# Kernel optimization log

Hardware: AMD Instinct MI355X
Metric: run time of the kernel (lower is better)

The kernel has to match this reference:

```python
import jax, jax.numpy as jnp
import numpy as np

N_NODES = 50000
N_EDGES = 800000
D_IN = 128
D_HID = 128
D_OUT = 128
N_GRAPHS = 512


def _linear_params(key, d_in, d_out):
    kw, kb = jax.random.split(key)
    bound = 1.0 / np.sqrt(d_in)
    W = jax.random.uniform(kw, (d_in, d_out), minval=-bound, maxval=bound, dtype=jnp.float32)
    b = jax.random.uniform(kb, (d_out,), minval=-bound, maxval=bound, dtype=jnp.float32)
    return W, b


def setup_inputs() -> dict:
    key = jax.random.key(0)
    ks = jax.random.split(key, 8)
    x = jax.random.normal(ks[0], (N_NODES, D_IN), dtype=jnp.float32)
    edge_index = jax.random.randint(ks[1], (2, N_EDGES), 0, N_NODES, dtype=jnp.int64)
    batch = jnp.sort(jax.random.randint(ks[2], (N_NODES,), 0, N_GRAPHS, dtype=jnp.int64))
    W1a, b1a = _linear_params(ks[3], D_IN, D_HID)
    W1b, b1b = _linear_params(ks[4], D_HID, D_HID)
    W2a, b2a = _linear_params(ks[5], D_HID, D_HID)
    W2b, b2b = _linear_params(ks[6], D_HID, D_OUT)
    Wfc, bfc = _linear_params(ks[7], D_OUT, D_OUT)
    return {"x": x, "edge_index": edge_index, "batch": batch,
            "W1a": W1a, "b1a": b1a, "W1b": W1b, "b1b": b1b,
            "W2a": W2a, "b2a": b2a, "W2b": W2b, "b2b": b2b,
            "Wfc": Wfc, "bfc": bfc}


def _gin_conv(h, src, dst, Wa, ba, Wb, bb):
    # neighbor sum: gather source features, scatter-add to targets (eps=0)
    agg = jax.ops.segment_sum(h[src], dst, num_segments=N_NODES)
    z = h + agg  # (1+eps)*x + sum_neighbors, eps=0
    z = jax.nn.relu(z @ Wa + ba)
    return z @ Wb + bb


def reference(x, edge_index, batch, W1a, b1a, W1b, b1b, W2a, b2a, W2b, b2b, Wfc, bfc):
    src, dst = edge_index[0], edge_index[1]
    h = jax.nn.relu(_gin_conv(x, src, dst, W1a, b1a, W1b, b1b))
    h = jax.nn.relu(_gin_conv(h, src, dst, W2a, b2a, W2b, b2b))
    g = jax.ops.segment_sum(h, batch, num_segments=N_GRAPHS)  # global_add_pool
    return jax.nn.relu(g @ Wfc + bfc)
```

## Files before the change

### kernel.cpp

```cpp
#include <hip/hip_runtime.h>

#define N_NODES 50000
#define N_EDGES 800000
#define N_GRAPHS 512
#define CAP 48

typedef __bf16 bf16x8 __attribute__((ext_vector_type(8)));
typedef float f32x4 __attribute__((ext_vector_type(4)));
typedef unsigned short u16;
typedef unsigned int u32;

__device__ __forceinline__ u16 f2bf(float f) {
    union { float f; u32 i; } v; v.f = f;
    u32 r = v.i + 0x7fffu + ((v.i >> 16) & 1u);
    return (u16)(r >> 16);
}
__device__ __forceinline__ float bf2f(u16 u) {
    union { u32 i; float f; } v; v.i = ((u32)u) << 16; return v.f;
}

__global__ void k_prep(const int* __restrict__ ei, int* __restrict__ cnt, u16* __restrict__ slots,
                       const float* __restrict__ X, u16* __restrict__ XB,
                       const float* __restrict__ W1a, const float* __restrict__ W1b,
                       const float* __restrict__ W2a, const float* __restrict__ W2b,
                       u16* __restrict__ T1a, u16* __restrict__ T1b,
                       u16* __restrict__ T2a, u16* __restrict__ T2b,
                       int E, int n4) {
    int bid = blockIdx.x;
    if (bid < 3125) {
        int e = bid * 256 + threadIdx.x;
        if (e < E) {
            int s = ei[e];
            int d = ei[E + e];
            int p = atomicAdd(&cnt[d * 4], 1);
            if (p < CAP) slots[(size_t)d * CAP + p] = (u16)s;
        }
    } else if (bid < 9375) {
        int i = (bid - 3125) * 256 + threadIdx.x;
        if (i < n4) {
            float4 v = ((const float4*)X)[i];
            ushort4 o;
            o.x = f2bf(v.x); o.y = f2bf(v.y); o.z = f2bf(v.z); o.w = f2bf(v.w);
            ((ushort4*)XB)[i] = o;
        }
    } else {
        int b2 = bid - 9375;
        int widx = b2 >> 6;
        int i = (b2 & 63) * 256 + threadIdx.x;
        const float* W = widx == 0 ? W1a : widx == 1 ? W1b : widx == 2 ? W2a : W2b;
        u16* T = widx == 0 ? T1a : widx == 1 ? T1b : widx == 2 ? T2a : T2b;
        int k = i >> 7, n = i & 127;
        T[n * 128 + k] = f2bf(W[k * 128 + n]);
    }
}

__global__ void k_agg(const u16* __restrict__ X, const int* __restrict__ cnt,
                      const u16* __restrict__ slots, u16* __restrict__ Z, int N) {
    int wid = (blockIdx.x * blockDim.x + threadIdx.x) >> 6;
    if (wid >= N) return;
    int lane = threadIdx.x & 63;
    const u32* X2 = (const u32*)X;
    u32 v = X2[(size_t)wid * 64 + lane];
    float ax = bf2f((u16)(v & 0xffff));
    float ay = bf2f((u16)(v >> 16));
    int deg = cnt[wid * 4];
    if (deg > CAP) deg = CAP;
    int idx = (lane < deg) ? (int)slots[(size_t)wid * CAP + lane] : 0;
    int j = 0;
    for (; j + 16 <= deg; j += 16) {
        u32 t[16];
#pragma unroll
        for (int u = 0; u < 16; ++u)
            t[u] = X2[(size_t)__shfl(idx, j + u) * 64 + lane];
        float sx = 0.f, sy = 0.f;
#pragma unroll
        for (int u = 0; u < 16; ++u) {
            sx += bf2f((u16)(t[u] & 0xffff));
            sy += bf2f((u16)(t[u] >> 16));
        }
        ax += sx; ay += sy;
    }
    for (; j + 4 <= deg; j += 4) {
        u32 t0 = X2[(size_t)__shfl(idx, j    ) * 64 + lane];
        u32 t1 = X2[(size_t)__shfl(idx, j + 1) * 64 + lane];
        u32 t2 = X2[(size_t)__shfl(idx, j + 2) * 64 + lane];
        u32 t3 = X2[(size_t)__shfl(idx, j + 3) * 64 + lane];
        ax += bf2f((u16)(t0 & 0xffff)) + bf2f((u16)(t1 & 0xffff))
            + bf2f((u16)(t2 & 0xffff)) + bf2f((u16)(t3 & 0xffff));
        ay += bf2f((u16)(t0 >> 16)) + bf2f((u16)(t1 >> 16))
            + bf2f((u16)(t2 >> 16)) + bf2f((u16)(t3 >> 16));
    }
    for (; j < deg; ++j) {
        u32 u = X2[(size_t)__shfl(idx, j) * 64 + lane];
        ax += bf2f((u16)(u & 0xffff));
        ay += bf2f((u16)(u >> 16));
    }
    ((u32*)Z)[(size_t)wid * 64 + lane] = (((u32)f2bf(ay)) << 16) | (u32)f2bf(ax);
}

__global__ __launch_bounds__(256, 1)
void k_mlp(const u16* __restrict__ Z, const u16* __restrict__ WaT,
           const float* __restrict__ ba, const u16* __restrict__ WbT,
           const float* __restrict__ bb, u16* __restrict__ H, int N) {
    __shared__ u16 smZ[128 * 128];
    __shared__ u16 smW[128 * 128];
    uint4* smZ4 = (uint4*)smZ;
    uint4* smW4 = (uint4*)smW;

    const int tid = threadIdx.x;
    const int lane = tid & 63, wv = tid >> 6;
    const int q = lane >> 4, m = lane & 15;
    const int row0 = blockIdx.x * 128;

    for (int i = tid; i < 2048; i += 256) {
        int r = i >> 4, c4 = i & 15;
        smW4[r * 16 + (c4 ^ (r & 15))] = ((const uint4*)WaT)[i];
    }
    for (int i = tid; i < 2048; i += 256) {
        int r = i >> 4, c4 = i & 15;
        int gr = row0 + r;
        uint4 v = make_uint4(0u, 0u, 0u, 0u);
        if (gr < N) v = ((const uint4*)Z)[(size_t)gr * 16 + c4];
        smZ4[r * 16 + (c4 ^ (r & 15))] = v;
    }
    __syncthreads();

    f32x4 acc[2][8];
    for (int rt = 0; rt < 2; ++rt)
        for (int nt = 0; nt < 8; ++nt)
            acc[rt][nt] = (f32x4){0.f, 0.f, 0.f, 0.f};
    for (int kt = 0; kt < 4; ++kt) {
        bf16x8 a[2];
        for (int rt = 0; rt < 2; ++rt) {
            int r = wv * 32 + rt * 16 + m;
            a[rt] = *(const bf16x8*)(smZ4 + (r * 16 + ((kt * 4 + q) ^ (r & 15))));
        }
        for (int nt = 0; nt < 8; ++nt) {
            int n = nt * 16 + m;
            bf16x8 bfr = *(const bf16x8*)(smW4 + (n * 16 + ((kt * 4 + q) ^ (n & 15))));
            for (int rt = 0; rt < 2; ++rt)
                acc[rt][nt] = __builtin_amdgcn_mfma_f32_16x16x32_bf16(a[rt], bfr, acc[rt][nt], 0, 0, 0);
        }
    }
    __syncthreads();

    for (int i = tid; i < 2048; i += 256) {
        int r = i >> 4, c4 = i & 15;
        smW4[r * 16 + (c4 ^ (r & 15))] = ((const uint4*)WbT)[i];
    }
    for (int nt = 0; nt < 8; ++nt) {
        int col = nt * 16 + m;
        float bias = ba[col];
        int c4 = col >> 3, ci = col & 7;
        for (int rt = 0; rt < 2; ++rt)
            for (int r2 = 0; r2 < 4; ++r2) {
                int row = wv * 32 + rt * 16 + q * 4 + r2;
                float x = acc[rt][nt][r2] + bias;
                x = x > 0.f ? x : 0.f;
                smZ[(row * 16 + (c4 ^ (row & 15))) * 8 + ci] = f2bf(x);
            }
    }
    __syncthreads();

    f32x4 acc2[2][8];
    for (int rt = 0; rt < 2; ++rt)
        for (int nt = 0; nt < 8; ++nt)
            acc2[rt][nt] = (f32x4){0.f, 0.f, 0.f, 0.f};
    for (int kt = 0; kt < 4; ++kt) {
        bf16x8 a[2];
        for (int rt = 0; rt < 2; ++rt) {
            int r = wv * 32 + rt * 16 + m;
            a[rt] = *(const bf16x8*)(smZ4 + (r * 16 + ((kt * 4 + q) ^ (r & 15))));
        }
        for (int nt = 0; nt < 8; ++nt) {
            int n = nt * 16 + m;
            bf16x8 bfr = *(const bf16x8*)(smW4 + (n * 16 + ((kt * 4 + q) ^ (n & 15))));
            for (int rt = 0; rt < 2; ++rt)
                acc2[rt][nt] = __builtin_amdgcn_mfma_f32_16x16x32_bf16(a[rt], bfr, acc2[rt][nt], 0, 0, 0);
        }
    }
    for (int nt = 0; nt < 8; ++nt) {
        int col = nt * 16 + m;
        float bias = bb[col];
        for (int rt = 0; rt < 2; ++rt)
            for (int r2 = 0; r2 < 4; ++r2) {
                int row = row0 + wv * 32 + rt * 16 + q * 4 + r2;
                if (row < N) {
                    float x = acc2[rt][nt][r2] + bias;
                    H[(size_t)row * 128 + col] = f2bf(x > 0.f ? x : 0.f);
                }
            }
    }
}

__global__ __launch_bounds__(256, 1)
void k_mlp2(const u16* __restrict__ Z, const u16* __restrict__ WaT,
            const float* __restrict__ ba, const u16* __restrict__ WbT,
            const float* __restrict__ bb, const int* __restrict__ batch,
            float* __restrict__ G, int N) {
    __shared__ u16 smZ[128 * 128];
    __shared__ u16 smW[128 * 128];
    __shared__ int sb[128];
    uint4* smZ4 = (uint4*)smZ;
    uint4* smW4 = (uint4*)smW;

    const int tid = threadIdx.x;
    const int lane = tid & 63, wv = tid >> 6;
    const int q = lane >> 4, m = lane & 15;
    const int row0 = blockIdx.x * 128;

    if (tid < 128) sb[tid] = (row0 + tid < N) ? batch[row0 + tid] : -1;

    for (int i = tid; i < 2048; i += 256) {
        int r = i >> 4, c4 = i & 15;
        smW4[r * 16 + (c4 ^ (r & 15))] = ((const uint4*)WaT)[i];
    }
    for (int i = tid; i < 2048; i += 256) {
        int r = i >> 4, c4 = i & 15;
        int gr = row0 + r;
        uint4 v = make_uint4(0u, 0u, 0u, 0u);
        if (gr < N) v = ((const uint4*)Z)[(size_t)gr * 16 + c4];
        smZ4[r * 16 + (c4 ^ (r & 15))] = v;
    }
    __syncthreads();

    f32x4 acc[2][8];
    for (int rt = 0; rt < 2; ++rt)
        for (int nt = 0; nt < 8; ++nt)
            acc[rt][nt] = (f32x4){0.f, 0.f, 0.f, 0.f};
    for (int kt = 0; kt < 4; ++kt) {
        bf16x8 a[2];
        for (int rt = 0; rt < 2; ++rt) {
            int r = wv * 32 + rt * 16 + m;
            a[rt] = *(const bf16x8*)(smZ4 + (r * 16 + ((kt * 4 + q) ^ (r & 15))));
        }
        for (int nt = 0; nt < 8; ++nt) {
            int n = nt * 16 + m;
            bf16x8 bfr = *(const bf16x8*)(smW4 + (n * 16 + ((kt * 4 + q) ^ (n & 15))));
            for (int rt = 0; rt < 2; ++rt)
                acc[rt][nt] = __builtin_amdgcn_mfma_f32_16x16x32_bf16(a[rt], bfr, acc[rt][nt], 0, 0, 0);
        }
    }
    __syncthreads();

    for (int i = tid; i < 2048; i += 256) {
        int r = i >> 4, c4 = i & 15;
        smW4[r * 16 + (c4 ^ (r & 15))] = ((const uint4*)WbT)[i];
    }
    for (int nt = 0; nt < 8; ++nt) {
        int col = nt * 16 + m;
        float bias = ba[col];
        int c4 = col >> 3, ci = col & 7;
        for (int rt = 0; rt < 2; ++rt)
            for (int r2 = 0; r2 < 4; ++r2) {
                int row = wv * 32 + rt * 16 + q * 4 + r2;
                float x = acc[rt][nt][r2] + bias;
                x = x > 0.f ? x : 0.f;
                smZ[(row * 16 + (c4 ^ (row & 15))) * 8 + ci] = f2bf(x);
            }
    }
    __syncthreads();

    f32x4 acc2[2][8];
    for (int rt = 0; rt < 2; ++rt)
        for (int nt = 0; nt < 8; ++nt)
            acc2[rt][nt] = (f32x4){0.f, 0.f, 0.f, 0.f};
    for (int kt = 0; kt < 4; ++kt) {
        bf16x8 a[2];
        for (int rt = 0; rt < 2; ++rt) {
            int r = wv * 32 + rt * 16 + m;
            a[rt] = *(const bf16x8*)(smZ4 + (r * 16 + ((kt * 4 + q) ^ (r & 15))));
        }
        for (int nt = 0; nt < 8; ++nt) {
            int n = nt * 16 + m;
            bf16x8 bfr = *(const bf16x8*)(smW4 + (n * 16 + ((kt * 4 + q) ^ (n & 15))));
            for (int rt = 0; rt < 2; ++rt)
                acc2[rt][nt] = __builtin_amdgcn_mfma_f32_16x16x32_bf16(a[rt], bfr, acc2[rt][nt], 0, 0, 0);
        }
    }
    for (int nt = 0; nt < 8; ++nt) {
        int col = nt * 16 + m;
        float bias = bb[col];
        for (int rt = 0; rt < 2; ++rt)
#pragma unroll
            for (int r2 = 0; r2 < 4; ++r2) {
                int row = wv * 32 + rt * 16 + q * 4 + r2;
                float x = acc2[rt][nt][r2] + bias;
                smZ[row * 128 + col] = f2bf(x > 0.f ? x : 0.f);
            }
    }
    __syncthreads();
    {
        int col = tid & 127, half = tid >> 7;
        int rbeg = half * 64, rend = rbeg + 64;
        float run = 0.f; int curg = -1;
        for (int r = rbeg; r < rend; ++r) {
            int gg = sb[r];
            if (gg < 0) break;
            if (gg != curg) {
                if (curg >= 0) atomicAdd(&G[curg * 128 + col], run);
                run = 0.f; curg = gg;
            }
            run += bf2f(smZ[r * 128 + col]);
        }
        if (curg >= 0) atomicAdd(&G[curg * 128 + col], run);
    }
}

__global__ void k_fc(const float* __restrict__ G, const float* __restrict__ W,
                     const float* __restrict__ bias, float* __restrict__ O) {
    __shared__ float gs[128];
    int t = threadIdx.x, gidx = blockIdx.x;
    gs[t] = G[gidx * 128 + t];
    __syncthreads();
    float acc = bias[t];
    for (int k = 0; k < 128; ++k)
        acc += gs[k] * W[k * 128 + t];
    acc = acc > 0.f ? acc : 0.f;
    O[gidx * 128 + t] = acc;
}

extern "C" void kernel_launch(void* const* d_in, const int* in_sizes, int n_in,
                              void* d_out, int out_size, void* d_ws, size_t ws_size,
                              hipStream_t stream) {
    const int N = N_NODES, E = N_EDGES, NG = N_GRAPHS;

    const float* x   = (const float*)d_in[0];
    const int* ei    = (const int*)d_in[1];
    const int* batch = (const int*)d_in[2];
    const float* W1a = (const float*)d_in[3];
    const float* b1a = (const float*)d_in[4];
    const float* W1b = (const float*)d_in[5];
    const float* b1b = (const float*)d_in[6];
    const float* W2a = (const float*)d_in[7];
    const float* b2a = (const float*)d_in[8];
    const float* W2b = (const float*)d_in[9];
    const float* b2b = (const float*)d_in[10];
    const float* Wfc = (const float*)d_in[11];
    const float* bfc = (const float*)d_in[12];
    float* out = (float*)d_out;

    char* w = (char*)d_ws;
    int* cnt    = (int*)(w + 0x0000000);
    float* g    = (float*)(w + 0x00C4000);
    u16* slots  = (u16*)(w + 0x0110000);
    u16* xb     = (u16*)(w + 0x05B0000);
    u16* zb     = (u16*)(w + 0x1280000);
    u16* hb     = (u16*)(w + 0x1F50000);
    u16* T1a    = (u16*)(w + 0x2C20000);
    u16* T1b    = (u16*)(w + 0x2C28000);
    u16* T2a    = (u16*)(w + 0x2C30000);
    u16* T2b    = (u16*)(w + 0x2C38000);

    (void)hipMemsetAsync(w, 0, 0x104000, stream);

    const int n4 = N * 128 / 4;
    k_prep<<<9631, 256, 0, stream>>>(ei, cnt, slots, x, xb, W1a, W1b, W2a, W2b,
                                     T1a, T1b, T2a, T2b, E, n4);

    const int AGGB = (N * 64 + 255) / 256;
    const int MLPB = (N + 127) / 128;

    k_agg<<<AGGB, 256, 0, stream>>>(xb, cnt, slots, zb, N);
    k_mlp<<<MLPB, 256, 0, stream>>>(zb, T1a, b1a, T1b, b1b, hb, N);
    k_agg<<<AGGB, 256, 0, stream>>>(hb, cnt, slots, xb, N);
    k_mlp2<<<MLPB, 256, 0, stream>>>(xb, T2a, b2a, T2b, b2b, batch, g, N);

    k_fc<<<NG, 128, 0, stream>>>(g, Wfc, bfc, out);
}
```

Measured before the change: 236.3 us.

## Fuse neighbor aggregation into the MLP kernels, writing aggregates straight to shared memory

Each GIN layer's gather/sum aggregation now runs inside the MLP kernel. Each wave aggregates 32 rows and writes the bf16 result into the swizzled shared-memory Z tile, so the intermediate Z buffer is no longer written to and re-read from global memory, and two launches go away. Launch bounds are raised to 2 blocks per CU to help hide gather latency. In exchange, parallelism in the gather phase drops: only 4 waves per 128-row block, processed serially, versus one wave per node before. This may expose gather latency.

Result: slower. 320.2 us (+35.5%).

```diff
diff --git a/kernel.cpp b/kernel.cpp
--- a/kernel.cpp
+++ b/kernel.cpp
@@ -54,74 +54,72 @@
     }
 }
 
-__global__ void k_agg(const u16* __restrict__ X, const int* __restrict__ cnt,
-                      const u16* __restrict__ slots, u16* __restrict__ Z, int N) {
-    int wid = (blockIdx.x * blockDim.x + threadIdx.x) >> 6;
-    if (wid >= N) return;
-    int lane = threadIdx.x & 63;
-    const u32* X2 = (const u32*)X;
-    u32 v = X2[(size_t)wid * 64 + lane];
-    float ax = bf2f((u16)(v & 0xffff));
-    float ay = bf2f((u16)(v >> 16));
-    int deg = cnt[wid * 4];
-    if (deg > CAP) deg = CAP;
-    int idx = (lane < deg) ? (int)slots[(size_t)wid * CAP + lane] : 0;
-    int j = 0;
-    for (; j + 16 <= deg; j += 16) {
-        u32 t[16];
-#pragma unroll
-        for (int u = 0; u < 16; ++u)
-            t[u] = X2[(size_t)__shfl(idx, j + u) * 64 + lane];
-        float sx = 0.f, sy = 0.f;
-#pragma unroll
-        for (int u = 0; u < 16; ++u) {
-            sx += bf2f((u16)(t[u] & 0xffff));
-            sy += bf2f((u16)(t[u] >> 16));
-        }
-        ax += sx; ay += sy;
-    }
-    for (; j + 4 <= deg; j += 4) {
-        u32 t0 = X2[(size_t)__shfl(idx, j    ) * 64 + lane];
-        u32 t1 = X2[(size_t)__shfl(idx, j + 1) * 64 + lane];
-        u32 t2 = X2[(size_t)__shfl(idx, j + 2) * 64 + lane];
-        u32 t3 = X2[(size_t)__shfl(idx, j + 3) * 64 + lane];
-        ax += bf2f((u16)(t0 & 0xffff)) + bf2f((u16)(t1 & 0xffff))
-            + bf2f((u16)(t2 & 0xffff)) + bf2f((u16)(t3 & 0xffff));
-        ay += bf2f((u16)(t0 >> 16)) + bf2f((u16)(t1 >> 16))
-            + bf2f((u16)(t2 >> 16)) + bf2f((u16)(t3 >> 16));
-    }
-    for (; j < deg; ++j) {
-        u32 u = X2[(size_t)__shfl(idx, j) * 64 + lane];
-        ax += bf2f((u16)(u & 0xffff));
-        ay += bf2f((u16)(u >> 16));
-    }
-    ((u32*)Z)[(size_t)wid * 64 + lane] = (((u32)f2bf(ay)) << 16) | (u32)f2bf(ax);
-}
-
-__global__ __launch_bounds__(256, 1)
-void k_mlp(const u16* __restrict__ Z, const u16* __restrict__ WaT,
-           const float* __restrict__ ba, const u16* __restrict__ WbT,
-           const float* __restrict__ bb, u16* __restrict__ H, int N) {
+__global__ __launch_bounds__(256, 2)
+void k_gin1(const u16* __restrict__ X, const int* __restrict__ cnt,
+            const u16* __restrict__ slots,
+            const u16* __restrict__ WaT, const float* __restrict__ ba,
+            const u16* __restrict__ WbT, const float* __restrict__ bb,
+            u16* __restrict__ H, int N) {
     __shared__ u16 smZ[128 * 128];
     __shared__ u16 smW[128 * 128];
     uint4* smZ4 = (uint4*)smZ;
     uint4* smW4 = (uint4*)smW;
+    u32* smZu = (u32*)smZ;
 
     const int tid = threadIdx.x;
     const int lane = tid & 63, wv = tid >> 6;
     const int q = lane >> 4, m = lane & 15;
     const int row0 = blockIdx.x * 128;
+    const u32* X2 = (const u32*)X;
 
     for (int i = tid; i < 2048; i += 256) {
         int r = i >> 4, c4 = i & 15;
         smW4[r * 16 + (c4 ^ (r & 15))] = ((const uint4*)WaT)[i];
     }
-    for (int i = tid; i < 2048; i += 256) {
-        int r = i >> 4, c4 = i & 15;
+
+    for (int i = 0; i < 32; ++i) {
+        int r = wv * 32 + i;
         int gr = row0 + r;
-        uint4 v = make_uint4(0u, 0u, 0u, 0u);
-        if (gr < N) v = ((const uint4*)Z)[(size_t)gr * 16 + c4];
-        smZ4[r * 16 + (c4 ^ (r & 15))] = v;
+        float ax = 0.f, ay = 0.f;
+        if (gr < N) {
+            u32 v = X2[(size_t)gr * 64 + lane];
+            ax = bf2f((u16)(v & 0xffff));
+            ay = bf2f((u16)(v >> 16));
+            int deg = cnt[gr * 4];
+            if (deg > CAP) deg = CAP;
+            int idx = (lane < deg) ? (int)slots[(size_t)gr * CAP + lane] : 0;
+            int j = 0;
+            for (; j + 16 <= deg; j += 16) {
+                u32 t[16];
+#pragma unroll
+                for (int u = 0; u < 16; ++u)
+                    t[u] = X2[(size_t)__shfl(idx, j + u) * 64 + lane];
+                float sx = 0.f, sy = 0.f;
+#pragma unroll
+                for (int u = 0; u < 16; ++u) {
+                    sx += bf2f((u16)(t[u] & 0xffff));
+                    sy += bf2f((u16)(t[u] >> 16));
+                }
+                ax += sx; ay += sy;
+            }
+            for (; j + 4 <= deg; j += 4) {
+                u32 t0 = X2[(size_t)__shfl(idx, j    ) * 64 + lane];
+                u32 t1 = X2[(size_t)__shfl(idx, j + 1) * 64 + lane];
+                u32 t2 = X2[(size_t)__shfl(idx, j + 2) * 64 + lane];
+                u32 t3 = X2[(size_t)__shfl(idx, j + 3) * 64 + lane];
+                ax += bf2f((u16)(t0 & 0xffff)) + bf2f((u16)(t1 & 0xffff))
+                    + bf2f((u16)(t2 & 0xffff)) + bf2f((u16)(t3 & 0xffff));
+                ay += bf2f((u16)(t0 >> 16)) + bf2f((u16)(t1 >> 16))
+                    + bf2f((u16)(t2 >> 16)) + bf2f((u16)(t3 >> 16));
+            }
+            for (; j < deg; ++j) {
+                u32 u = X2[(size_t)__shfl(idx, j) * 64 + lane];
+                ax += bf2f((u16)(u & 0xffff));
+                ay += bf2f((u16)(u >> 16));
+            }
+        }
+        smZu[(r * 16 + ((lane >> 2) ^ (r & 15))) * 4 + (lane & 3)] =
+            (((u32)f2bf(ay)) << 16) | (u32)f2bf(ax);
     }
     __syncthreads();
 
@@ -193,21 +191,24 @@
     }
 }
 
-__global__ __launch_bounds__(256, 1)
-void k_mlp2(const u16* __restrict__ Z, const u16* __restrict__ WaT,
-            const float* __restrict__ ba, const u16* __restrict__ WbT,
-            const float* __restrict__ bb, const int* __restrict__ batch,
-            float* __restrict__ G, int N) {
+__global__ __launch_bounds__(256, 2)
+void k_gin2(const u16* __restrict__ X, const int* __restrict__ cnt,
+            const u16* __restrict__ slots,
+            const u16* __restrict__ WaT, const float* __restrict__ ba,
+            const u16* __restrict__ WbT, const float* __restrict__ bb,
+            const int* __restrict__ batch, float* __restrict__ G, int N) {
     __shared__ u16 smZ[128 * 128];
     __shared__ u16 smW[128 * 128];
     __shared__ int sb[128];
     uint4* smZ4 = (uint4*)smZ;
     uint4* smW4 = (uint4*)smW;
+    u32* smZu = (u32*)smZ;
 
     const int tid = threadIdx.x;
     const int lane = tid & 63, wv = tid >> 6;
     const int q = lane >> 4, m = lane & 15;
     const int row0 = blockIdx.x * 128;
+    const u32* X2 = (const u32*)X;
 
     if (tid < 128) sb[tid] = (row0 + tid < N) ? batch[row0 + tid] : -1;
 
@@ -215,12 +216,50 @@
         int r = i >> 4, c4 = i & 15;
         smW4[r * 16 + (c4 ^ (r & 15))] = ((const uint4*)WaT)[i];
     }
-    for (int i = tid; i < 2048; i += 256) {
-        int r = i >> 4, c4 = i & 15;
+
+    for (int i = 0; i < 32; ++i) {
+        int r = wv * 32 + i;
         int gr = row0 + r;
-        uint4 v = make_uint4(0u, 0u, 0u, 0u);
-        if (gr < N) v = ((const uint4*)Z)[(size_t)gr * 16 + c4];
-        smZ4[r * 16 + (c4 ^ (r & 15))] = v;
+        float ax = 0.f, ay = 0.f;
+        if (gr < N) {
+            u32 v = X2[(size_t)gr * 64 + lane];
+            ax = bf2f((u16)(v & 0xffff));
+            ay = bf2f((u16)(v >> 16));
+            int deg = cnt[gr * 4];
+            if (deg > CAP) deg = CAP;
+            int idx = (lane < deg) ? (int)slots[(size_t)gr * CAP + lane] : 0;
+            int j = 0;
+            for (; j + 16 <= deg; j += 16) {
+                u32 t[16];
+#pragma unroll
+                for (int u = 0; u < 16; ++u)
+                    t[u] = X2[(size_t)__shfl(idx, j + u) * 64 + lane];
+                float sx = 0.f, sy = 0.f;
+#pragma unroll
+                for (int u = 0; u < 16; ++u) {
+                    sx += bf2f((u16)(t[u] & 0xffff));
+                    sy += bf2f((u16)(t[u] >> 16));
+                }
+                ax += sx; ay += sy;
+            }
+            for (; j + 4 <= deg; j += 4) {
+                u32 t0 = X2[(size_t)__shfl(idx, j    ) * 64 + lane];
+                u32 t1 = X2[(size_t)__shfl(idx, j + 1) * 64 + lane];
+                u32 t2 = X2[(size_t)__shfl(idx, j + 2) * 64 + lane];
+                u32 t3 = X2[(size_t)__shfl(idx, j + 3) * 64 + lane];
+                ax += bf2f((u16)(t0 & 0xffff)) + bf2f((u16)(t1 & 0xffff))
+                    + bf2f((u16)(t2 & 0xffff)) + bf2f((u16)(t3 & 0xffff));
+                ay += bf2f((u16)(t0 >> 16)) + bf2f((u16)(t1 >> 16))
+                    + bf2f((u16)(t2 >> 16)) + bf2f((u16)(t3 >> 16));
+            }
+            for (; j < deg; ++j) {
+                u32 u = X2[(size_t)__shfl(idx, j) * 64 + lane];
+                ax += bf2f((u16)(u & 0xffff));
+                ay += bf2f((u16)(u >> 16));
+            }
+        }
+        smZu[(r * 16 + ((lane >> 2) ^ (r & 15))) * 4 + (lane & 3)] =
+            (((u32)f2bf(ay)) << 16) | (u32)f2bf(ax);
     }
     __syncthreads();
 
@@ -345,7 +384,6 @@
     float* g    = (float*)(w + 0x00C4000);
     u16* slots  = (u16*)(w + 0x0110000);
     u16* xb     = (u16*)(w + 0x05B0000);
-    u16* zb     = (u16*)(w + 0x1280000);
     u16* hb     = (u16*)(w + 0x1F50000);
     u16* T1a    = (u16*)(w + 0x2C20000);
     u16* T1b    = (u16*)(w + 0x2C28000);
@@ -358,13 +396,10 @@
     k_prep<<<9631, 256, 0, stream>>>(ei, cnt, slots, x, xb, W1a, W1b, W2a, W2b,
                                      T1a, T1b, T2a, T2b, E, n4);
 
-    const int AGGB = (N * 64 + 255) / 256;
     const int MLPB = (N + 127) / 128;
 
-    k_agg<<<AGGB, 256, 0, stream>>>(xb, cnt, slots, zb, N);
-    k_mlp<<<MLPB, 256, 0, stream>>>(zb, T1a, b1a, T1b, b1b, hb, N);
-    k_agg<<<AGGB, 256, 0, stream>>>(hb, cnt, slots, xb, N);
-    k_mlp2<<<MLPB, 256, 0, stream>>>(xb, T2a, b2a, T2b, b2b, batch, g, N);
+    k_gin1<<<MLPB, 256, 0, stream>>>(xb, cnt, slots, T1a, b1a, T1b, b1b, hb, N);
+    k_gin2<<<MLPB, 256, 0, stream>>>(hb, cnt, slots, T2a, b2a, T2b, b2b, batch, g, N);
 
     k_fc<<<NG, 128, 0, stream>>>(g, Wfc, bfc, out);
 }
```

## Fuse neighbor aggregation into MLP kernels with double-buffered gathers per block

Applied to the files above, without the earlier changes.

Merges the separate aggregation and MLP kernels into one per GIN layer. Each 512-thread block handles 64 rows: it gathers neighbor indices into shared memory, accumulates them with double-buffered 16-wide gathers, writes the aggregated rows straight into the shared Z tile, then runs both MFMA GEMMs. A zero sentinel row is appended to the feature buffers so padded index slots add zero instead of needing branches. This removes the round trip of the intermediate aggregate through global memory and two kernel launches, at the cost of more shared memory and register pressure per block and an MLP tile shrunk from 128 to 64 rows.

New measurement: 229.9 us. 2.7% less time.

```diff
diff --git a/kernel.cpp b/kernel.cpp
--- a/kernel.cpp
+++ b/kernel.cpp
@@ -4,6 +4,7 @@
 #define N_EDGES 800000
 #define N_GRAPHS 512
 #define CAP 48
+#define ZN N_NODES
 
 typedef __bf16 bf16x8 __attribute__((ext_vector_type(8)));
 typedef float f32x4 __attribute__((ext_vector_type(4)));
@@ -20,7 +21,7 @@
 }
 
 __global__ void k_prep(const int* __restrict__ ei, int* __restrict__ cnt, u16* __restrict__ slots,
-                       const float* __restrict__ X, u16* __restrict__ XB,
+                       const float* __restrict__ X, u16* __restrict__ XB, u16* __restrict__ HB,
                        const float* __restrict__ W1a, const float* __restrict__ W1b,
                        const float* __restrict__ W2a, const float* __restrict__ W2b,
                        u16* __restrict__ T1a, u16* __restrict__ T1b,
@@ -43,7 +44,7 @@
             o.x = f2bf(v.x); o.y = f2bf(v.y); o.z = f2bf(v.z); o.w = f2bf(v.w);
             ((ushort4*)XB)[i] = o;
         }
-    } else {
+    } else if (bid < 9631) {
         int b2 = bid - 9375;
         int widx = b2 >> 6;
         int i = (b2 & 63) * 256 + threadIdx.x;
@@ -51,248 +52,276 @@
         u16* T = widx == 0 ? T1a : widx == 1 ? T1b : widx == 2 ? T2a : T2b;
         int k = i >> 7, n = i & 127;
         T[n * 128 + k] = f2bf(W[k * 128 + n]);
-    }
-}
-
-__global__ void k_agg(const u16* __restrict__ X, const int* __restrict__ cnt,
-                      const u16* __restrict__ slots, u16* __restrict__ Z, int N) {
-    int wid = (blockIdx.x * blockDim.x + threadIdx.x) >> 6;
-    if (wid >= N) return;
-    int lane = threadIdx.x & 63;
-    const u32* X2 = (const u32*)X;
-    u32 v = X2[(size_t)wid * 64 + lane];
-    float ax = bf2f((u16)(v & 0xffff));
-    float ay = bf2f((u16)(v >> 16));
-    int deg = cnt[wid * 4];
-    if (deg > CAP) deg = CAP;
-    int idx = (lane < deg) ? (int)slots[(size_t)wid * CAP + lane] : 0;
-    int j = 0;
-    for (; j + 16 <= deg; j += 16) {
-        u32 t[16];
-#pragma unroll
-        for (int u = 0; u < 16; ++u)
-            t[u] = X2[(size_t)__shfl(idx, j + u) * 64 + lane];
-        float sx = 0.f, sy = 0.f;
-#pragma unroll
-        for (int u = 0; u < 16; ++u) {
-            sx += bf2f((u16)(t[u] & 0xffff));
-            sy += bf2f((u16)(t[u] >> 16));
-        }
-        ax += sx; ay += sy;
-    }
-    for (; j + 4 <= deg; j += 4) {
-        u32 t0 = X2[(size_t)__shfl(idx, j    ) * 64 + lane];
-        u32 t1 = X2[(size_t)__shfl(idx, j + 1) * 64 + lane];
-        u32 t2 = X2[(size_t)__shfl(idx, j + 2) * 64 + lane];
-        u32 t3 = X2[(size_t)__shfl(idx, j + 3) * 64 + lane];
-        ax += bf2f((u16)(t0 & 0xffff)) + bf2f((u16)(t1 & 0xffff))
-            + bf2f((u16)(t2 & 0xffff)) + bf2f((u16)(t3 & 0xffff));
-        ay += bf2f((u16)(t0 >> 16)) + bf2f((u16)(t1 >> 16))
-            + bf2f((u16)(t2 >> 16)) + bf2f((u16)(t3 >> 16));
-    }
-    for (; j < deg; ++j) {
-        u32 u = X2[(size_t)__shfl(idx, j) * 64 + lane];
-        ax += bf2f((u16)(u & 0xffff));
-        ay += bf2f((u16)(u >> 16));
-    }
-    ((u32*)Z)[(size_t)wid * 64 + lane] = (((u32)f2bf(ay)) << 16) | (u32)f2bf(ax);
-}
-
-__global__ __launch_bounds__(256, 1)
-void k_mlp(const u16* __restrict__ Z, const u16* __restrict__ WaT,
-           const float* __restrict__ ba, const u16* __restrict__ WbT,
-           const float* __restrict__ bb, u16* __restrict__ H, int N) {
-    __shared__ u16 smZ[128 * 128];
+    } else {
+        int t = threadIdx.x;
+        if (t < 64)       ((u32*)XB)[(size_t)ZN * 64 + t]        = 0u;
+        else if (t < 128) ((u32*)HB)[(size_t)ZN * 64 + (t - 64)] = 0u;
+    }
+}
+
+
+#define STAGE16(BUF, CI, CJ)                                            \
+    _Pragma("unroll")                                                   \
+    for (int u = 0; u < 16; ++u) {                                      \
+        u32 nb = (u32)smI[wv][(CI)][(CJ) + u];                          \
+        BUF[u] = X2[(nb << 6) + lane];                                  \
+    }
+
+#define ACCUM16(BUF)                                                    \
+    _Pragma("unroll")                                                   \
+    for (int u = 0; u < 16; ++u) {                                      \
+        ax += bf2f((u16)(BUF[u] & 0xffff));                             \
+        ay += bf2f((u16)(BUF[u] >> 16));                                \
+    }
+
+#define FINROW(CI) {                                                    \
+        int r = wv * 8 + (CI);                                          \
+        smZu[(r * 16 + ((lane >> 2) ^ (r & 15))) * 4 + (lane & 3)] =    \
+            (((u32)f2bf(ay)) << 16) | (u32)f2bf(ax);                    \
+        ax = 0.f; ay = 0.f;                                             \
+    }
+
+#define AGG_PHASE()                                                                  \
+    int degv = 0;                                                                    \
+    {                                                                                \
+        int gr = row0 + wv * 8 + lane;                                               \
+        if (lane < 8 && gr < N) {                                                    \
+            int d = cnt[gr * 4];                                                     \
+            degv = d > CAP ? CAP : d;                                                \
+        }                                                                            \
+    }                                                                                \
+    {                                                                                \
+        u32 tv[8];                                                                   \
+        int sl = lane - 1; sl = sl < 0 ? 0 : (sl >= CAP ? CAP - 1 : sl);             \
+        _Pragma("unroll")                                                            \
+        for (int i = 0; i < 8; ++i) {                                                \
+            int gr = row0 + wv * 8 + i;                                              \
+            tv[i] = (gr < N) ? (u32)slots[(size_t)gr * CAP + sl] : (u32)ZN;          \
+        }                                                                            \
+        _Pragma("unroll")                                                            \
+        for (int i = 0; i < 8; ++i) {                                                \
+            int gr = row0 + wv * 8 + i;                                              \
+            int de = __builtin_amdgcn_readlane(degv, i) + 1;                         \
+            u32 v = (lane == 0) ? (u32)gr : tv[i];                                   \
+            if (gr >= N || lane >= de) v = ZN;                                       \
+            smI[wv][i][lane] = (u16)v;                                               \
+        }                                                                            \
+    }                                                                                \
+    {                                                                                \
+        float ax = 0.f, ay = 0.f;                                                    \
+        u32 bufA[16], bufB[16];                                                      \
+        int ci = 0, cj = 0;                                                          \
+        int de = __builtin_amdgcn_readlane(degv, 0) + 1;                             \
+        STAGE16(bufA, 0, 0);                                                         \
+        for (;;) {                                                                   \
+            int ni = ci, nj = cj + 16;                                               \
+            if (nj >= de) { ni = ci + 1; nj = 0; }                                   \
+            int have = (ni < 8);                                                     \
+            if (have) { de = __builtin_amdgcn_readlane(degv, ni) + 1;                \
+                        STAGE16(bufB, ni, nj); }                                     \
+            ACCUM16(bufA);                                                           \
+            if (nj == 0) FINROW(ci);                                                 \
+            if (!have) break;                                                        \
+            ci = ni; cj = nj;                                                        \
+            ni = ci; nj = cj + 16;                                                   \
+            if (nj >= de) { ni = ci + 1; nj = 0; }                                   \
+            have = (ni < 8);                                                         \
+            if (have) { de = __builtin_amdgcn_readlane(degv, ni) + 1;                \
+                        STAGE16(bufA, ni, nj); }                                     \
+            ACCUM16(bufB);                                                           \
+            if (nj == 0) FINROW(ci);                                                 \
+            if (!have) break;                                                        \
+            ci = ni; cj = nj;                                                        \
+        }                                                                            \
+    }
+
+__global__ __launch_bounds__(512, 4)
+void k_gin1(const u16* __restrict__ X, const int* __restrict__ cnt,
+            const u16* __restrict__ slots,
+            const u16* __restrict__ WaT, const float* __restrict__ ba,
+            const u16* __restrict__ WbT, const float* __restrict__ bb,
+            u16* __restrict__ H, int N) {
+    __shared__ u16 smZ[64 * 128];
     __shared__ u16 smW[128 * 128];
+    __shared__ u16 smI[8][8][64];
     uint4* smZ4 = (uint4*)smZ;
     uint4* smW4 = (uint4*)smW;
+    u32* smZu = (u32*)smZ;
 
     const int tid = threadIdx.x;
     const int lane = tid & 63, wv = tid >> 6;
     const int q = lane >> 4, m = lane & 15;
-    const int row0 = blockIdx.x * 128;
-
-    for (int i = tid; i < 2048; i += 256) {
+    const int ws = wv & 3, wc = wv >> 2;
+    const int row0 = blockIdx.x * 64;
+    const u32* X2 = (const u32*)X;
+
+    for (int i = tid; i < 2048; i += 512) {
         int r = i >> 4, c4 = i & 15;
         smW4[r * 16 + (c4 ^ (r & 15))] = ((const uint4*)WaT)[i];
     }
-    for (int i = tid; i < 2048; i += 256) {
-        int r = i >> 4, c4 = i & 15;
-        int gr = row0 + r;
-        uint4 v = make_uint4(0u, 0u, 0u, 0u);
-        if (gr < N) v = ((const uint4*)Z)[(size_t)gr * 16 + c4];
-        smZ4[r * 16 + (c4 ^ (r & 15))] = v;
-    }
-    __syncthreads();
-
-    f32x4 acc[2][8];
-    for (int rt = 0; rt < 2; ++rt)
-        for (int nt = 0; nt < 8; ++nt)
-            acc[rt][nt] = (f32x4){0.f, 0.f, 0.f, 0.f};
+
+    AGG_PHASE();
+    __syncthreads();
+
+    f32x4 acc[4];
+#pragma unroll
+    for (int nt = 0; nt < 4; ++nt) acc[nt] = (f32x4){0.f, 0.f, 0.f, 0.f};
+#pragma unroll
     for (int kt = 0; kt < 4; ++kt) {
-        bf16x8 a[2];
-        for (int rt = 0; rt < 2; ++rt) {
-            int r = wv * 32 + rt * 16 + m;
-            a[rt] = *(const bf16x8*)(smZ4 + (r * 16 + ((kt * 4 + q) ^ (r & 15))));
-        }
-        for (int nt = 0; nt < 8; ++nt) {
-            int n = nt * 16 + m;
+        int r = ws * 16 + m;
+        bf16x8 a = *(const bf16x8*)(smZ4 + (r * 16 + ((kt * 4 + q) ^ (r & 15))));
+#pragma unroll
+        for (int nt = 0; nt < 4; ++nt) {
+            int n = (wc * 4 + nt) * 16 + m;
             bf16x8 bfr = *(const bf16x8*)(smW4 + (n * 16 + ((kt * 4 + q) ^ (n & 15))));
-            for (int rt = 0; rt < 2; ++rt)
-                acc[rt][nt] = __builtin_amdgcn_mfma_f32_16x16x32_bf16(a[rt], bfr, acc[rt][nt], 0, 0, 0);
-        }
-    }
-    __syncthreads();
-
-    for (int i = tid; i < 2048; i += 256) {
+            acc[nt] = __builtin_amdgcn_mfma_f32_16x16x32_bf16(a, bfr, acc[nt], 0, 0, 0);
+        }
+    }
+    __syncthreads();
+
+    for (int i = tid; i < 2048; i += 512) {
         int r = i >> 4, c4 = i & 15;
         smW4[r * 16 + (c4 ^ (r & 15))] = ((const uint4*)WbT)[i];
     }
-    for (int nt = 0; nt < 8; ++nt) {
-        int col = nt * 16 + m;
+#pragma unroll
+    for (int nt = 0; nt < 4; ++nt) {
+        int col = (wc * 4 + nt) * 16 + m;
         float bias = ba[col];
-        int c4 = col >> 3, ci = col & 7;
-        for (int rt = 0; rt < 2; ++rt)
-            for (int r2 = 0; r2 < 4; ++r2) {
-                int row = wv * 32 + rt * 16 + q * 4 + r2;
-                float x = acc[rt][nt][r2] + bias;
-                x = x > 0.f ? x : 0.f;
-                smZ[(row * 16 + (c4 ^ (row & 15))) * 8 + ci] = f2bf(x);
+        int c4 = col >> 3, ci8 = col & 7;
+#pragma unroll
+        for (int r2 = 0; r2 < 4; ++r2) {
+            int row = ws * 16 + q * 4 + r2;
+            float x = acc[nt][r2] + bias;
+            x = x > 0.f ? x : 0.f;
+            smZ[(row * 16 + (c4 ^ (row & 15))) * 8 + ci8] = f2bf(x);
+        }
+    }
+    __syncthreads();
+
+    f32x4 acc2[4];
+#pragma unroll
+    for (int nt = 0; nt < 4; ++nt) acc2[nt] = (f32x4){0.f, 0.f, 0.f, 0.f};
+#pragma unroll
+    for (int kt = 0; kt < 4; ++kt) {
+        int r = ws * 16 + m;
+        bf16x8 a = *(const bf16x8*)(smZ4 + (r * 16 + ((kt * 4 + q) ^ (r & 15))));
+#pragma unroll
+        for (int nt = 0; nt < 4; ++nt) {
+            int n = (wc * 4 + nt) * 16 + m;
+            bf16x8 bfr = *(const bf16x8*)(smW4 + (n * 16 + ((kt * 4 + q) ^ (n & 15))));
+            acc2[nt] = __builtin_amdgcn_mfma_f32_16x16x32_bf16(a, bfr, acc2[nt], 0, 0, 0);
+        }
+    }
+#pragma unroll
+    for (int nt = 0; nt < 4; ++nt) {
+        int col = (wc * 4 + nt) * 16 + m;
+        float bias = bb[col];
+#pragma unroll
+        for (int r2 = 0; r2 < 4; ++r2) {
+            int row = row0 + ws * 16 + q * 4 + r2;
+            if (row < N) {
+                float x = acc2[nt][r2] + bias;
+                H[(size_t)row * 128 + col] = f2bf(x > 0.f ? x : 0.f);
             }
-    }
-    __syncthreads();
-
-    f32x4 acc2[2][8];
-    for (int rt = 0; rt < 2; ++rt)
-        for (int nt = 0; nt < 8; ++nt)
-            acc2[rt][nt] = (f32x4){0.f, 0.f, 0.f, 0.f};
-    for (int kt = 0; kt < 4; ++kt) {
-        bf16x8 a[2];
-        for (int rt = 0; rt < 2; ++rt) {
-            int r = wv * 32 + rt * 16 + m;
-            a[rt] = *(const bf16x8*)(smZ4 + (r * 16 + ((kt * 4 + q) ^ (r & 15))));
-        }
-        for (int nt = 0; nt < 8; ++nt) {
-            int n = nt * 16 + m;
-            bf16x8 bfr = *(const bf16x8*)(smW4 + (n * 16 + ((kt * 4 + q) ^ (n & 15))));
-            for (int rt = 0; rt < 2; ++rt)
-                acc2[rt][nt] = __builtin_amdgcn_mfma_f32_16x16x32_bf16(a[rt], bfr, acc2[rt][nt], 0, 0, 0);
-        }
-    }
-    for (int nt = 0; nt < 8; ++nt) {
-        int col = nt * 16 + m;
-        float bias = bb[col];
-        for (int rt = 0; rt < 2; ++rt)
-            for (int r2 = 0; r2 < 4; ++r2) {
-                int row = row0 + wv * 32 + rt * 16 + q * 4 + r2;
-                if (row < N) {
-                    float x = acc2[rt][nt][r2] + bias;
-                    H[(size_t)row * 128 + col] = f2bf(x > 0.f ? x : 0.f);
-                }
-            }
-    }
-}
-
-__global__ __launch_bounds__(256, 1)
-void k_mlp2(const u16* __restrict__ Z, const u16* __restrict__ WaT,
-            const float* __restrict__ ba, const u16* __restrict__ WbT,
-            const float* __restrict__ bb, const int* __restrict__ batch,
-            float* __restrict__ G, int N) {
-    __shared__ u16 smZ[128 * 128];
+        }
+    }
+}
+
+__global__ __launch_bounds__(512, 4)
+void k_gin2(const u16* __restrict__ X, const int* __restrict__ cnt,
+            const u16* __restrict__ slots,
+            const u16* __restrict__ WaT, const float* __restrict__ ba,
+            const u16* __restrict__ WbT, const float* __restrict__ bb,
+            const int* __restrict__ batch, float* __restrict__ G, int N) {
+    __shared__ u16 smZ[64 * 128];
     __shared__ u16 smW[128 * 128];
-    __shared__ int sb[128];
+    __shared__ u16 smI[8][8][64];
+    __shared__ int sb[64];
     uint4* smZ4 = (uint4*)smZ;
     uint4* smW4 = (uint4*)smW;
+    u32* smZu = (u32*)smZ;
 
     const int tid = threadIdx.x;
     const int lane = tid & 63, wv = tid >> 6;
     const int q = lane >> 4, m = lane & 15;
-    const int row0 = blockIdx.x * 128;
-
-    if (tid < 128) sb[tid] = (row0 + tid < N) ? batch[row0 + tid] : -1;
-
-    for (int i = tid; i < 2048; i += 256) {
+    const int ws = wv & 3, wc = wv >> 2;
+    const int row0 = blockIdx.x * 64;
+    const u32* X2 = (const u32*)X;
+
+    if (tid < 64) sb[tid] = (row0 + tid < N) ? batch[row0 + tid] : -1;
+
+    for (int i = tid; i < 2048; i += 512) {
         int r = i >> 4, c4 = i & 15;
         smW4[r * 16 + (c4 ^ (r & 15))] = ((const uint4*)WaT)[i];
     }
-    for (int i = tid; i < 2048; i += 256) {
-        int r = i >> 4, c4 = i & 15;
-        int gr = row0 + r;
-        uint4 v = make_uint4(0u, 0u, 0u, 0u);
-        if (gr < N) v = ((const uint4*)Z)[(size_t)gr * 16 + c4];
-        smZ4[r * 16 + (c4 ^ (r & 15))] = v;
-    }
-    __syncthreads();
-
-    f32x4 acc[2][8];
-    for (int rt = 0; rt < 2; ++rt)
-        for (int nt = 0; nt < 8; ++nt)
-            acc[rt][nt] = (f32x4){0.f, 0.f, 0.f, 0.f};
+
+    AGG_PHASE();
+    __syncthreads();
+
+    f32x4 acc[4];
+#pragma unroll
+    for (int nt = 0; nt < 4; ++nt) acc[nt] = (f32x4){0.f, 0.f, 0.f, 0.f};
+#pragma unroll
     for (int kt = 0; kt < 4; ++kt) {
-        bf16x8 a[2];
-        for (int rt = 0; rt < 2; ++rt) {
-            int r = wv * 32 + rt * 16 + m;
-            a[rt] = *(const bf16x8*)(smZ4 + (r * 16 + ((kt * 4 + q) ^ (r & 15))));
-        }
-        for (int nt = 0; nt < 8; ++nt) {
-            int n = nt * 16 + m;
+        int r = ws * 16 + m;
+        bf16x8 a = *(const bf16x8*)(smZ4 + (r * 16 + ((kt * 4 + q) ^ (r & 15))));
+#pragma unroll
+        for (int nt = 0; nt < 4; ++nt) {
+            int n = (wc * 4 + nt) * 16 + m;
             bf16x8 bfr = *(const bf16x8*)(smW4 + (n * 16 + ((kt * 4 + q) ^ (n & 15))));
-            for (int rt = 0; rt < 2; ++rt)
-                acc[rt][nt] = __builtin_amdgcn_mfma_f32_16x16x32_bf16(a[rt], bfr, acc[rt][nt], 0, 0, 0);
-        }
-    }
-    __syncthreads();
-
-    for (int i = tid; i < 2048; i += 256) {
+            acc[nt] = __builtin_amdgcn_mfma_f32_16x16x32_bf16(a, bfr, acc[nt], 0, 0, 0);
+        }
+    }
+    __syncthreads();
+
+    for (int i = tid; i < 2048; i += 512) {
         int r = i >> 4, c4 = i & 15;
         smW4[r * 16 + (c4 ^ (r & 15))] = ((const uint4*)WbT)[i];
     }
-    for (int nt = 0; nt < 8; ++nt) {
-        int col = nt * 16 + m;
+#pragma unroll
+    for (int nt = 0; nt < 4; ++nt) {
+        int col = (wc * 4 + nt) * 16 + m;
         float bias = ba[col];
-        int c4 = col >> 3, ci = col & 7;
-        for (int rt = 0; rt < 2; ++rt)
-            for (int r2 = 0; r2 < 4; ++r2) {
-                int row = wv * 32 + rt * 16 + q * 4 + r2;
-                float x = acc[rt][nt][r2] + bias;
-                x = x > 0.f ? x : 0.f;
-                smZ[(row * 16 + (c4 ^ (row & 15))) * 8 + ci] = f2bf(x);
-            }
-    }
-    __syncthreads();
-
-    f32x4 acc2[2][8];
-    for (int rt = 0; rt < 2; ++rt)
-        for (int nt = 0; nt < 8; ++nt)
-            acc2[rt][nt] = (f32x4){0.f, 0.f, 0.f, 0.f};
+        int c4 = col >> 3, ci8 = col & 7;
+#pragma unroll
+        for (int r2 = 0; r2 < 4; ++r2) {
+            int row = ws * 16 + q * 4 + r2;
+            float x = acc[nt][r2] + bias;
+            x = x > 0.f ? x : 0.f;
+            smZ[(row * 16 + (c4 ^ (row & 15))) * 8 + ci8] = f2bf(x);
+        }
+    }
+    __syncthreads();
+
+    f32x4 acc2[4];
+#pragma unroll
+    for (int nt = 0; nt < 4; ++nt) acc2[nt] = (f32x4){0.f, 0.f, 0.f, 0.f};
+#pragma unroll
     for (int kt = 0; kt < 4; ++kt) {
-        bf16x8 a[2];
-        for (int rt = 0; rt < 2; ++rt) {
-            int r = wv * 32 + rt * 16 + m;
-            a[rt] = *(const bf16x8*)(smZ4 + (r * 16 + ((kt * 4 + q) ^ (r & 15))));
-        }
-        for (int nt = 0; nt < 8; ++nt) {
-            int n = nt * 16 + m;
+        int r = ws * 16 + m;
+        bf16x8 a = *(const bf16x8*)(smZ4 + (r * 16 + ((kt * 4 + q) ^ (r & 15))));
+#pragma unroll
+        for (int nt = 0; nt < 4; ++nt) {
+            int n = (wc * 4 + nt) * 16 + m;
             bf16x8 bfr = *(const bf16x8*)(smW4 + (n * 16 + ((kt * 4 + q) ^ (n & 15))));
-            for (int rt = 0; rt < 2; ++rt)
-                acc2[rt][nt] = __builtin_amdgcn_mfma_f32_16x16x32_bf16(a[rt], bfr, acc2[rt][nt], 0, 0, 0);
-        }
-    }
-    for (int nt = 0; nt < 8; ++nt) {
-        int col = nt * 16 + m;
+            acc2[nt] = __builtin_amdgcn_mfma_f32_16x16x32_bf16(a, bfr, acc2[nt], 0, 0, 0);
+        }
+    }
+#pragma unroll
+    for (int nt = 0; nt < 4; ++nt) {
+        int col = (wc * 4 + nt) * 16 + m;
         float bias = bb[col];
-        for (int rt = 0; rt < 2; ++rt)
-#pragma unroll
-            for (int r2 = 0; r2 < 4; ++r2) {
-                int row = wv * 32 + rt * 16 + q * 4 + r2;
-                float x = acc2[rt][nt][r2] + bias;
-                smZ[row * 128 + col] = f2bf(x > 0.f ? x : 0.f);
-            }
+#pragma unroll
+        for (int r2 = 0; r2 < 4; ++r2) {
+            int row = ws * 16 + q * 4 + r2;
+            float x = acc2[nt][r2] + bias;
+            smZ[row * 128 + col] = f2bf(x > 0.f ? x : 0.f);
+        }
     }
     __syncthreads();
     {
-        int col = tid & 127, half = tid >> 7;
-        int rbeg = half * 64, rend = rbeg + 64;
+        int col = tid & 127, quarter = tid >> 7;
+        int rbeg = quarter * 16, rend = rbeg + 16;
         float run = 0.f; int curg = -1;
         for (int r = rbeg; r < rend; ++r) {
             int gg = sb[r];
@@ -345,7 +374,6 @@
     float* g    = (float*)(w + 0x00C4000);
     u16* slots  = (u16*)(w + 0x0110000);
     u16* xb     = (u16*)(w + 0x05B0000);
-    u16* zb     = (u16*)(w + 0x1280000);
     u16* hb     = (u16*)(w + 0x1F50000);
     u16* T1a    = (u16*)(w + 0x2C20000);
     u16* T1b    = (u16*)(w + 0x2C28000);
@@ -355,16 +383,13 @@
     (void)hipMemsetAsync(w, 0, 0x104000, stream);
 
     const int n4 = N * 128 / 4;
-    k_prep<<<9631, 256, 0, stream>>>(ei, cnt, slots, x, xb, W1a, W1b, W2a, W2b,
+    k_prep<<<9632, 256, 0, stream>>>(ei, cnt, slots, x, xb, hb, W1a, W1b, W2a, W2b,
                                      T1a, T1b, T2a, T2b, E, n4);
 
-    const int AGGB = (N * 64 + 255) / 256;
-    const int MLPB = (N + 127) / 128;
-
-    k_agg<<<AGGB, 256, 0, stream>>>(xb, cnt, slots, zb, N);
-    k_mlp<<<MLPB, 256, 0, stream>>>(zb, T1a, b1a, T1b, b1b, hb, N);
-    k_agg<<<AGGB, 256, 0, stream>>>(hb, cnt, slots, xb, N);
-    k_mlp2<<<MLPB, 256, 0, stream>>>(xb, T2a, b2a, T2b, b2b, batch, g, N);
+    const int GINB = (N + 63) / 64;
+
+    k_gin1<<<GINB, 512, 0, stream>>>(xb, cnt, slots, T1a, b1a, T1b, b1b, hb, N);
+    k_gin2<<<GINB, 512, 0, stream>>>(hb, cnt, slots, T2a, b2a, T2b, b2b, batch, g, N);
 
     k_fc<<<NG, 128, 0, stream>>>(g, Wfc, bfc, out);
 }
```
